# Kernel optimization log

Hardware: AMD Instinct MI355X
Metric: run time of the kernel (lower is better)

## Reference

```python
import jax, jax.numpy as jnp
import numpy as np

D_MODEL = 64  # angle_dist_dim
IN_CH = 256
EPS = 1e-6


def sinusoidal_embedding(e, d_model):
    # e: (N, K) -> (N, K, d_model), interleaved [sin0, cos0, sin1, cos1, ...]
    div_term = jnp.exp(jnp.arange(0, d_model, 2, dtype=jnp.float32) * (-np.log(10000.0) / d_model))
    om = e[..., None] * div_term  # (N, K, d_model//2)
    emb = jnp.stack([jnp.sin(om), jnp.cos(om)], axis=-1)  # (N, K, d/2, 2)
    return emb.reshape(e.shape + (d_model,))


def setup_inputs() -> dict:
    key = jax.random.key(0)
    ks = jax.random.split(key, 5)
    N, K, C = 40000, 16, IN_CH
    triplet_dim = 2 * C + D_MODEL  # 576
    x = jax.random.normal(ks[0], (N, C), dtype=jnp.float32)
    pos = jax.random.normal(ks[1], (N, 3), dtype=jnp.float32) * 10.0
    anchor_indices = jnp.arange(N, dtype=jnp.int32)
    corner_indices = jax.random.randint(ks[2], (N, K, 2), 0, N, dtype=jnp.int32)
    corner_masks = jnp.ones((N, K), dtype=bool)
    Wqkv_w = jax.random.normal(ks[3], (3 * C, triplet_dim), dtype=jnp.float32) / np.sqrt(triplet_dim)
    Wqkv_b = jax.random.normal(ks[4], (3 * C,), dtype=jnp.float32) * 0.01
    return {"x": x, "pos": pos, "anchor_indices": anchor_indices,
            "corner_indices": corner_indices, "corner_masks": corner_masks,
            "Wqkv_w": Wqkv_w, "Wqkv_b": Wqkv_b}


def reference(x, pos, anchor_indices, corner_indices, corner_masks, Wqkv_w, Wqkv_b):
    N, C = x.shape
    padded_x = jnp.concatenate([x, jnp.zeros((1, C), x.dtype)], axis=0)
    padded_pos = jnp.concatenate([pos, jnp.zeros((1, 3), pos.dtype)], axis=0)

    anchor_p = padded_pos[anchor_indices]            # (Na, 3)
    v0 = padded_pos[corner_indices[:, :, 0]] - anchor_p[:, None]  # (Na, K, 3)
    v1 = padded_pos[corner_indices[:, :, 1]] - anchor_p[:, None]
    v0 = jax.lax.stop_gradient(v0).at[:, :, 2].set(0.0)  # zero z (detached geometry)
    v1 = jax.lax.stop_gradient(v1).at[:, :, 2].set(0.0)

    cos_values = jnp.sum(v0 * v1, axis=-1) / (
        jnp.linalg.norm(v0, axis=-1) * jnp.linalg.norm(v1, axis=-1) + EPS)
    # z-component of cross product (x,y only since z was zeroed)
    sin_z = v0[..., 0] * v1[..., 1] - v0[..., 1] * v1[..., 0]
    reorder = sin_z < 0  # (Na, K)

    ci = jnp.where(reorder[..., None], corner_indices[:, :, ::-1], corner_indices)

    nv0 = jax.lax.stop_gradient(padded_pos[ci[:, :, 0]] - anchor_p[:, None]).at[:, :, 2].set(0.0)
    nv1 = jax.lax.stop_gradient(padded_pos[ci[:, :, 1]] - anchor_p[:, None]).at[:, :, 2].set(0.0)
    new_sin_z = nv0[..., 0] * nv1[..., 1] - nv0[..., 1] * nv1[..., 0]
    # corner_masks is all-True so boolean selection == full flatten (static shape)
    triplet_false_masks = ((new_sin_z < -1e-6) & corner_masks).reshape(-1)

    angle_features = jax.lax.stop_gradient(sinusoidal_embedding(cos_values, D_MODEL))
    triplet_feats = jnp.concatenate(
        [padded_x[ci[:, :, 0]], padded_x[ci[:, :, 1]], angle_features], axis=-1)  # (Na, K, 576)

    qkv = triplet_feats @ Wqkv_w.T + Wqkv_b            # (Na, K, 3C)
    qkv = qkv.reshape(qkv.shape[0], qkv.shape[1], 3, C)
    q, k, v = qkv[:, :, 0], qkv[:, :, 1], qkv[:, :, 2]

    scores = jnp.einsum('nqc,nkc->nqk', q, k) / np.sqrt(C)
    attn = jax.nn.softmax(scores, axis=-1)
    attn_feats = jnp.einsum('nqk,nkc->nqc', attn, v)   # (Na, K, C)

    mask_f = corner_masks.astype(attn_feats.dtype)
    denom = jnp.sum(mask_f, axis=1, keepdims=True)     # (Na, 1)
    mean_feats = jnp.sum(attn_feats * mask_f[..., None], axis=1) / denom  # (Na, C)

    x_messages = jnp.zeros_like(x).at[anchor_indices].set(mean_feats)
    out = jnp.concatenate([x, x_messages], axis=1)     # (N, 2C), triplet_mlp_method='concat'
    return out, triplet_false_masks
```

## Files before the change

kernel.cpp:

```cpp
#include <hip/hip_runtime.h>

typedef unsigned short u16;
typedef __attribute__((ext_vector_type(8))) short short8v;
typedef __attribute__((ext_vector_type(4))) float float4v;

__device__ __forceinline__ float bf2f(u16 u) {
  union { unsigned int i; float f; } v; v.i = ((unsigned int)u) << 16; return v.f;
}
__device__ __forceinline__ u16 f2bf(float f) {
  union { unsigned int i; float f; } v; v.f = f;
  unsigned int r = v.i + 0x7fffu + ((v.i >> 16) & 1u);
  return (u16)(r >> 16);
}
__device__ __forceinline__ float4v mfma_bf16(short8v a, short8v b, float4v c) {
  return __builtin_amdgcn_mfma_f32_16x16x32_bf16(a, b, c, 0, 0, 0);
}

__global__ __launch_bounds__(256) void prep_kernel(const float* __restrict__ W,
                                                   u16* __restrict__ Bt,
                                                   u16* __restrict__ W2t) {
  int j = blockIdx.x;
  int c = threadIdx.x;
  const float* wr = W + (size_t)j * 576;
  Bt[(size_t)j * 256 + c]         = f2bf(wr[c]);
  Bt[(size_t)(768 + j) * 256 + c] = f2bf(wr[256 + c]);
  if (c < 64) W2t[(size_t)j * 64 + c] = f2bf(wr[512 + c]);
}

__global__ __launch_bounds__(256) void gemm_kernel(const float* __restrict__ A,
                                                   const u16* __restrict__ Bt,
                                                   u16* __restrict__ Y, int M) {
  __shared__ __align__(16) u16 As[128][72];
  __shared__ __align__(16) u16 Bs[128][72];
  int tid = threadIdx.x;
  int row0 = blockIdx.x * 128, col0 = blockIdx.y * 128;
  int w = tid >> 6, l = tid & 63;
  int wr = w >> 1, wc = w & 1;
  int lr = l & 15, lq = l >> 4;

  float4v acc[4][4];
#pragma unroll
  for (int mi = 0; mi < 4; mi++)
#pragma unroll
    for (int ni = 0; ni < 4; ni++) acc[mi][ni] = (float4v)0.f;

  for (int k0 = 0; k0 < 256; k0 += 64) {
#pragma unroll
    for (int i = 0; i < 4; i++) {
      int chunk = tid + i * 256;
      int r = chunk >> 3;
      int kc = (chunk & 7) * 8;
      int gr = row0 + r;
      short8v av = (short8v)0;
      if (gr < M) {
        float4 f0 = *(const float4*)(A + (size_t)gr * 256 + k0 + kc);
        float4 f1 = *(const float4*)(A + (size_t)gr * 256 + k0 + kc + 4);
        av[0] = (short)f2bf(f0.x); av[1] = (short)f2bf(f0.y);
        av[2] = (short)f2bf(f0.z); av[3] = (short)f2bf(f0.w);
        av[4] = (short)f2bf(f1.x); av[5] = (short)f2bf(f1.y);
        av[6] = (short)f2bf(f1.z); av[7] = (short)f2bf(f1.w);
      }
      *(short8v*)&As[r][kc] = av;
      short8v bv = *(const short8v*)(Bt + (size_t)(col0 + r) * 256 + k0 + kc);
      *(short8v*)&Bs[r][kc] = bv;
    }
    __syncthreads();
#pragma unroll
    for (int s = 0; s < 2; s++) {
      int kb = s * 32 + lq * 8;
      short8v af[4], bf[4];
#pragma unroll
      for (int mi = 0; mi < 4; mi++)
        af[mi] = *(const short8v*)&As[wr * 64 + mi * 16 + lr][kb];
#pragma unroll
      for (int ni = 0; ni < 4; ni++)
        bf[ni] = *(const short8v*)&Bs[wc * 64 + ni * 16 + lr][kb];
#pragma unroll
      for (int mi = 0; mi < 4; mi++)
#pragma unroll
        for (int ni = 0; ni < 4; ni++)
          acc[mi][ni] = mfma_bf16(af[mi], bf[ni], acc[mi][ni]);
    }
    __syncthreads();
  }
#pragma unroll
  for (int mi = 0; mi < 4; mi++)
#pragma unroll
    for (int ni = 0; ni < 4; ni++) {
      int rbase = row0 + wr * 64 + mi * 16 + lq * 4;
      int c = col0 + wc * 64 + ni * 16 + lr;
#pragma unroll
      for (int j = 0; j < 4; j++) {
        int r = rbase + j;
        if (r < M) Y[(size_t)r * 1536 + c] = f2bf(acc[mi][ni][j]);
      }
    }
}

__global__ __launch_bounds__(64) void triplet_kernel(
    const float* __restrict__ x, const float* __restrict__ pos,
    const int* __restrict__ anchor, const int* __restrict__ corner,
    const float* __restrict__ bias, const u16* __restrict__ Y,
    const u16* __restrict__ W2t, float* __restrict__ out, int N) {
  __shared__ float s_cos[16];
  __shared__ int s_i0[16], s_i1[16];
  __shared__ __align__(16) u16 s_qkv[16][776];

  int n = blockIdx.x;
  if (n >= N) return;
  int l = threadIdx.x;
  int lr = l & 15, lq = l >> 4, kg = lq * 8;
  int a = anchor[n];

  if (l < 16) {
    int t = l;
    int2 ci = ((const int2*)corner)[n * 16 + t];
    float ax = pos[(size_t)a * 3], ay = pos[(size_t)a * 3 + 1];
    float v0x = pos[(size_t)ci.x * 3]     - ax;
    float v0y = pos[(size_t)ci.x * 3 + 1] - ay;
    float v1x = pos[(size_t)ci.y * 3]     - ax;
    float v1y = pos[(size_t)ci.y * 3 + 1] - ay;
    float dot = v0x * v1x + v0y * v1y;
    float n0 = sqrtf(v0x * v0x + v0y * v0y);
    float n1 = sqrtf(v1x * v1x + v1y * v1y);
    s_cos[t] = dot / (n0 * n1 + 1e-6f);
    float sinz = v0x * v1y - v0y * v1x;
    bool sw = sinz < 0.f;
    s_i0[t] = sw ? ci.y : ci.x;
    s_i1[t] = sw ? ci.x : ci.y;
    out[(size_t)N * 512 + (size_t)n * 16 + t] = 0.0f;
  }
  {
    float4 v = ((const float4*)(x + (size_t)n * 256))[l];
    ((float4*)(out + (size_t)n * 512))[l] = v;
  }
  __syncthreads();

  float cosv = s_cos[lr];
  short8v a0, a1;
#pragma unroll
  for (int j = 0; j < 8; j++) {
    int k = kg + j;
    float dv0 = __expf(-0.28782313662425572f * (float)(k >> 1));
    float om0 = cosv * dv0;
    float f0 = (k & 1) ? __cosf(om0) : __sinf(om0);
    a0[j] = (short)f2bf(f0);
    int k2 = 32 + kg + j;
    float dv1 = __expf(-0.28782313662425572f * (float)(k2 >> 1));
    float om1 = cosv * dv1;
    float f1 = (k2 & 1) ? __cosf(om1) : __sinf(om1);
    a1[j] = (short)f2bf(f1);
  }
  int i0r[4], i1r[4];
#pragma unroll
  for (int j = 0; j < 4; j++) {
    int t = lq * 4 + j;
    i0r[j] = s_i0[t];
    i1r[j] = s_i1[t];
  }

  for (int nt = 0; nt < 48; nt++) {
    int col = nt * 16 + lr;
    short8v b0 = *(const short8v*)(W2t + (size_t)col * 64 + kg);
    short8v b1 = *(const short8v*)(W2t + (size_t)col * 64 + 32 + kg);
    float4v acc = (float4v)0.f;
    acc = mfma_bf16(a0, b0, acc);
    acc = mfma_bf16(a1, b1, acc);
    float bs = bias[col];
#pragma unroll
    for (int j = 0; j < 4; j++) {
      float v = acc[j] + bs + bf2f(Y[(size_t)i0r[j] * 1536 + col]) +
                bf2f(Y[(size_t)i1r[j] * 1536 + 768 + col]);
      s_qkv[lq * 4 + j][col] = f2bf(v);
    }
  }
  __syncthreads();

  float4v sa = (float4v)0.f;
#pragma unroll
  for (int cs = 0; cs < 8; cs++) {
    short8v qf = *(const short8v*)&s_qkv[lr][cs * 32 + kg];
    short8v kf = *(const short8v*)&s_qkv[lr][256 + cs * 32 + kg];
    sa = mfma_bf16(qf, kf, sa);
  }
  float wsum = 0.f;
#pragma unroll
  for (int j = 0; j < 4; j++) {
    float s = sa[j] * 0.0625f;
    float m = s;
    m = fmaxf(m, __shfl_xor(m, 1));
    m = fmaxf(m, __shfl_xor(m, 2));
    m = fmaxf(m, __shfl_xor(m, 4));
    m = fmaxf(m, __shfl_xor(m, 8));
    float e = __expf(s - m);
    float sm = e;
    sm += __shfl_xor(sm, 1);
    sm += __shfl_xor(sm, 2);
    sm += __shfl_xor(sm, 4);
    sm += __shfl_xor(sm, 8);
    wsum += e / sm;
  }
  wsum += __shfl_xor(wsum, 16);
  wsum += __shfl_xor(wsum, 32);
  wsum *= 0.0625f;

  float o0 = 0.f, o1 = 0.f, o2 = 0.f, o3 = 0.f;
#pragma unroll
  for (int kk = 0; kk < 16; kk++) {
    float wk = __shfl(wsum, kk);
    ushort4 v4 = *(const ushort4*)&s_qkv[kk][512 + l * 4];
    o0 += wk * bf2f(v4.x);
    o1 += wk * bf2f(v4.y);
    o2 += wk * bf2f(v4.z);
    o3 += wk * bf2f(v4.w);
  }
  float4 ov; ov.x = o0; ov.y = o1; ov.z = o2; ov.w = o3;
  ((float4*)(out + (size_t)a * 512 + 256))[l] = ov;
}

extern "C" void kernel_launch(void* const* d_in, const int* in_sizes, int n_in,
                              void* d_out, int out_size, void* d_ws, size_t ws_size,
                              hipStream_t stream) {
  const float* x    = (const float*)d_in[0];
  const float* pos  = (const float*)d_in[1];
  const int* anchor = (const int*)d_in[2];
  const int* corner = (const int*)d_in[3];
  const float* W    = (const float*)d_in[5];
  const float* bias = (const float*)d_in[6];
  float* out = (float*)d_out;
  int N = in_sizes[2];

  char* wsb = (char*)d_ws;
  u16* Bt  = (u16*)wsb;
  u16* W2t = (u16*)(wsb + 786432);
  u16* Y   = (u16*)(wsb + 786432 + 98304);

  prep_kernel<<<768, 256, 0, stream>>>(W, Bt, W2t);
  gemm_kernel<<<dim3((N + 127) / 128, 12), 256, 0, stream>>>(x, Bt, Y, N);
  triplet_kernel<<<N, 64, 0, stream>>>(x, pos, anchor, corner, bias, Y, W2t, out, N);
}
```

Baseline: 868.5 us.

## Transpose triplet MFMA to vectorize gathers and batch loads in flight

Swaps the MFMA operand order so each lane owns one triplet row and four consecutive output columns. This turns the scalar bf16 gathers from Y and the bias loads into 8-byte/16-byte vector loads, and the LDS stores into ushort4 writes. Loads for eight column tiles are issued before their MFMAs to raise memory-level parallelism. The sinusoid divisors are also precomputed once into shared memory instead of calling exp per element. The cost is higher register pressure from the batched buffers in a 64-thread block.

New measurement: 1.109 ms. +27.7%, slower.

```diff
diff --git a/kernel.cpp b/kernel.cpp
--- a/kernel.cpp
+++ b/kernel.cpp
@@ -103,6 +103,7 @@
     const float* __restrict__ bias, const u16* __restrict__ Y,
     const u16* __restrict__ W2t, float* __restrict__ out, int N) {
   __shared__ float s_cos[16];
+  __shared__ float s_div[32];
   __shared__ int s_i0[16], s_i1[16];
   __shared__ __align__(16) u16 s_qkv[16][776];
 
@@ -112,6 +113,7 @@
   int lr = l & 15, lq = l >> 4, kg = lq * 8;
   int a = anchor[n];
 
+  if (l < 32) s_div[l] = __expf(-0.28782313662425572f * (float)l);
   if (l < 16) {
     int t = l;
     int2 ci = ((const int2*)corner)[n * 16 + t];
@@ -139,39 +141,49 @@
   float cosv = s_cos[lr];
   short8v a0, a1;
 #pragma unroll
-  for (int j = 0; j < 8; j++) {
-    int k = kg + j;
-    float dv0 = __expf(-0.28782313662425572f * (float)(k >> 1));
-    float om0 = cosv * dv0;
-    float f0 = (k & 1) ? __cosf(om0) : __sinf(om0);
-    a0[j] = (short)f2bf(f0);
-    int k2 = 32 + kg + j;
-    float dv1 = __expf(-0.28782313662425572f * (float)(k2 >> 1));
-    float om1 = cosv * dv1;
-    float f1 = (k2 & 1) ? __cosf(om1) : __sinf(om1);
-    a1[j] = (short)f2bf(f1);
-  }
-  int i0r[4], i1r[4];
-#pragma unroll
-  for (int j = 0; j < 4; j++) {
-    int t = lq * 4 + j;
-    i0r[j] = s_i0[t];
-    i1r[j] = s_i1[t];
-  }
-
-  for (int nt = 0; nt < 48; nt++) {
-    int col = nt * 16 + lr;
-    short8v b0 = *(const short8v*)(W2t + (size_t)col * 64 + kg);
-    short8v b1 = *(const short8v*)(W2t + (size_t)col * 64 + 32 + kg);
-    float4v acc = (float4v)0.f;
-    acc = mfma_bf16(a0, b0, acc);
-    acc = mfma_bf16(a1, b1, acc);
-    float bs = bias[col];
-#pragma unroll
-    for (int j = 0; j < 4; j++) {
-      float v = acc[j] + bs + bf2f(Y[(size_t)i0r[j] * 1536 + col]) +
-                bf2f(Y[(size_t)i1r[j] * 1536 + 768 + col]);
-      s_qkv[lq * 4 + j][col] = f2bf(v);
+  for (int jj = 0; jj < 4; jj++) {
+    int kh = (kg >> 1) + jj;
+    float om0 = cosv * s_div[kh];
+    a0[2 * jj]     = (short)f2bf(__sinf(om0));
+    a0[2 * jj + 1] = (short)f2bf(__cosf(om0));
+    float om1 = cosv * s_div[16 + kh];
+    a1[2 * jj]     = (short)f2bf(__sinf(om1));
+    a1[2 * jj + 1] = (short)f2bf(__cosf(om1));
+  }
+
+  int t = lr;
+  const u16* y0p = Y + (size_t)s_i0[t] * 1536;
+  const u16* y1p = Y + (size_t)s_i1[t] * 1536 + 768;
+
+#pragma unroll 1
+  for (int nt0 = 0; nt0 < 48; nt0 += 8) {
+    short8v w0[8], w1[8];
+    ushort4 gy0[8], gy1[8];
+    float4 gb[8];
+#pragma unroll
+    for (int u = 0; u < 8; u++) {
+      int nt = nt0 + u;
+      const u16* wrp = W2t + (size_t)(nt * 16 + lr) * 64;
+      w0[u] = *(const short8v*)(wrp + kg);
+      w1[u] = *(const short8v*)(wrp + 32 + kg);
+      int c0 = nt * 16 + lq * 4;
+      gy0[u] = *(const ushort4*)(y0p + c0);
+      gy1[u] = *(const ushort4*)(y1p + c0);
+      gb[u]  = *(const float4*)(bias + c0);
+    }
+#pragma unroll
+    for (int u = 0; u < 8; u++) {
+      int nt = nt0 + u;
+      int c0 = nt * 16 + lq * 4;
+      float4v acc = (float4v)0.f;
+      acc = mfma_bf16(w0[u], a0, acc);
+      acc = mfma_bf16(w1[u], a1, acc);
+      ushort4 st;
+      st.x = f2bf(acc[0] + gb[u].x + bf2f(gy0[u].x) + bf2f(gy1[u].x));
+      st.y = f2bf(acc[1] + gb[u].y + bf2f(gy0[u].y) + bf2f(gy1[u].y));
+      st.z = f2bf(acc[2] + gb[u].z + bf2f(gy0[u].z) + bf2f(gy1[u].z));
+      st.w = f2bf(acc[3] + gb[u].w + bf2f(gy0[u].w) + bf2f(gy1[u].w));
+      *(ushort4*)&s_qkv[t][c0] = st;
     }
   }
   __syncthreads();
```
